# Performance work log

Hardware: AMD Instinct MI355X
Metric: run time of the kernel (lower is better)

The kernel has to match this reference:

```python
import jax, jax.numpy as jnp
import numpy as np

D_MODEL = 1024
NUM_HEADS = 16
DEPTH = D_MODEL // NUM_HEADS


def setup_inputs() -> dict:
    key = jax.random.key(0)
    ks = jax.random.split(key, 11)
    B, S = 2, 2048
    s = 1.0 / np.sqrt(D_MODEL)
    inp = {
        'query': jax.random.normal(ks[0], (B, S, D_MODEL), jnp.float32),
        'key': jax.random.normal(ks[1], (B, S, D_MODEL), jnp.float32),
        'value': jax.random.normal(ks[2], (B, S, D_MODEL), jnp.float32),
        'Wq': jax.random.normal(ks[3], (D_MODEL, D_MODEL), jnp.float32) * s,
        'bq': jnp.zeros((D_MODEL,), jnp.float32),
        'Wk': jax.random.normal(ks[4], (D_MODEL, D_MODEL), jnp.float32) * s,
        'bk': jnp.zeros((D_MODEL,), jnp.float32),
        'Wv': jax.random.normal(ks[5], (D_MODEL, D_MODEL), jnp.float32) * s,
        'bv': jnp.zeros((D_MODEL,), jnp.float32),
        'Wo': jax.random.normal(ks[6], (D_MODEL, D_MODEL), jnp.float32) * s,
        'bo': jnp.zeros((D_MODEL,), jnp.float32),
    }
    return inp


def reference(query, key, value, Wq, bq, Wk, bk, Wv, bv, Wo, bo):
    B, S, _ = query.shape
    # QKV projections (nn.Linear: x @ W.T + b; here W stored as [in,out])
    Q = query @ Wq + bq
    K = key @ Wk + bk
    V = value @ Wv + bv
    # [B, H, S, depth]
    Q = Q.reshape(B, S, NUM_HEADS, DEPTH).transpose(0, 2, 1, 3)
    K = K.reshape(B, S, NUM_HEADS, DEPTH).transpose(0, 2, 1, 3)
    V = V.reshape(B, S, NUM_HEADS, DEPTH).transpose(0, 2, 1, 3)
    scores = jnp.einsum('bhqd,bhkd->bhqk', Q, K) / jnp.sqrt(jnp.float32(DEPTH))
    weights = jax.nn.softmax(scores, axis=-1)
    out = jnp.einsum('bhqk,bhkd->bhqd', weights, V)
    out = out.transpose(0, 2, 1, 3).reshape(B, S, D_MODEL)
    return out @ Wo + bo
```

## Files before the change

kernel.cpp:

```cpp
#include <hip/hip_runtime.h>
#include <stdint.h>

#define D_MODEL 1024
#define NHEAD   16
#define DEPTH   64
#define BATCH   2
#define SEQ     2048
#define M_ROWS  (BATCH*SEQ)

typedef __attribute__((ext_vector_type(8))) short short8;
typedef __attribute__((ext_vector_type(4))) float f32x4;
typedef _Float16 __attribute__((ext_vector_type(8))) half8;
typedef __fp16 __attribute__((ext_vector_type(2))) fp16x2;

__device__ __forceinline__ unsigned short f2b(float f) {
    union { float f; uint32_t u; } v; v.f = f;
    uint32_t r = (v.u + 0x7FFFu + ((v.u >> 16) & 1u)) >> 16;
    return (unsigned short)r;
}
__device__ __forceinline__ unsigned short f2h(float f) {
    union { _Float16 h; unsigned short u; } c; c.h = (_Float16)f; return c.u;
}
__device__ __forceinline__ unsigned int pkh(float a, float b) {
    union { fp16x2 h; unsigned int u; } c;
    c.h = __builtin_amdgcn_cvt_pkrtz(a, b);
    return c.u;
}
__device__ __forceinline__ float exp2fast(float x) {
#if defined(__has_builtin) && __has_builtin(__builtin_amdgcn_exp2f)
    return __builtin_amdgcn_exp2f(x);
#else
    return exp2f(x);
#endif
}

__device__ __forceinline__ void glds16(const void* g, void* l) {
    __builtin_amdgcn_global_load_lds(
        (const __attribute__((address_space(1))) unsigned int*)(uintptr_t)g,
        (__attribute__((address_space(3))) unsigned int*)(unsigned int)(uintptr_t)l,
        16, 0, 0);
}

__global__ __launch_bounds__(256) void cast3_bf16(
    const float* __restrict__ s0, const float* __restrict__ s1, const float* __restrict__ s2,
    unsigned short* __restrict__ d0, unsigned short* __restrict__ d1, unsigned short* __restrict__ d2)
{
    const float* s; unsigned short* d;
    if (blockIdx.y == 0)      { s = s0; d = d0; }
    else if (blockIdx.y == 1) { s = s1; d = d1; }
    else                      { s = s2; d = d2; }
    int i = blockIdx.x * 256 + threadIdx.x;
    float4 v = ((const float4*)s)[i];
    ushort4 u;
    u.x = f2b(v.x); u.y = f2b(v.y); u.z = f2b(v.z); u.w = f2b(v.w);
    ((ushort4*)d)[i] = u;
}

__global__ __launch_bounds__(256) void transpose_w(
    const float* __restrict__ w0, const float* __restrict__ w1,
    const float* __restrict__ w2, const float* __restrict__ w3,
    unsigned short* __restrict__ t0, unsigned short* __restrict__ t1,
    unsigned short* __restrict__ t2, unsigned short* __restrict__ t3)
{
    __shared__ unsigned short tile[64][65];
    const float* w; unsigned short* t;
    const int z = blockIdx.z;
    switch (z) {
        case 0:  w = w0; t = t0; break;
        case 1:  w = w1; t = t1; break;
        case 2:  w = w2; t = t2; break;
        default: w = w3; t = t3; break;
    }
    const float sc = (z == 0) ? 0.125f * 1.44269504089f : 1.0f;
    const int k0 = blockIdx.y * 64;
    const int n0 = blockIdx.x * 64;
    const int tid = threadIdx.x;
    #pragma unroll
    for (int i = 0; i < 16; ++i) {
        int idx = i * 256 + tid;
        int r = idx >> 6, c = idx & 63;
        tile[c][r] = f2b(w[(size_t)(k0 + r) * D_MODEL + n0 + c] * sc);
    }
    __syncthreads();
    #pragma unroll
    for (int i = 0; i < 16; ++i) {
        int idx = i * 256 + tid;
        int r = idx >> 6, c = idx & 63;
        t[(size_t)(n0 + r) * D_MODEL + k0 + c] = tile[r][c];
    }
}

template<int OUT_MODE, bool BIAS_M>
__device__ __forceinline__ void gemm_body(
    const unsigned short* __restrict__ A, const unsigned short* __restrict__ Bt,
    const float* __restrict__ bias, float bscale, void* __restrict__ Cv,
    int m0, int n0, int N, int K, unsigned short* As, unsigned short* Bs)
{
    const int tid  = threadIdx.x;
    const int lane = tid & 63;
    const int wave = tid >> 6;
    const int wm = wave & 1, wn = wave >> 1;
    const int quad = lane >> 4, l16 = lane & 15;

    auto stage = [&](int buf, int k0) {
        unsigned short* Ad = As + buf * (128 * 32);
        unsigned short* Bd = Bs + buf * (128 * 32);
        #pragma unroll
        for (int i = 0; i < 2; ++i) {
            int c = i * 256 + tid;
            int row = c >> 2, cb = c & 3;
            glds16(A  + (size_t)(m0 + row) * K + k0 + cb * 8, Ad + c * 8);
            glds16(Bt + (size_t)(n0 + row) * K + k0 + cb * 8, Bd + c * 8);
        }
    };

    f32x4 acc[4][4] = {};
    float bn[4];
    if (!BIAS_M) {
        #pragma unroll
        for (int nt = 0; nt < 4; ++nt) bn[nt] = bias[n0 + wn * 64 + nt * 16 + l16] * bscale;
    }

    stage(0, 0);
    const int NIT = K / 32;
    for (int it = 0; it < NIT; ++it) {
        __syncthreads();
        const unsigned short* Ab = As + (it & 1) * (128 * 32);
        const unsigned short* Bb = Bs + (it & 1) * (128 * 32);
        if (it + 1 < NIT) stage((it + 1) & 1, (it + 1) * 32);
        short8 af[4], bg[4];
        #pragma unroll
        for (int t = 0; t < 4; ++t) {
            af[t] = *(const short8*)&Ab[(wm * 64 + t * 16 + l16) * 32 + quad * 8];
            bg[t] = *(const short8*)&Bb[(wn * 64 + t * 16 + l16) * 32 + quad * 8];
        }
        #pragma unroll
        for (int mt = 0; mt < 4; ++mt)
            #pragma unroll
            for (int nt = 0; nt < 4; ++nt)
                acc[mt][nt] = __builtin_amdgcn_mfma_f32_16x16x32_bf16(af[mt], bg[nt], acc[mt][nt], 0, 0, 0);
    }

    #pragma unroll
    for (int mt = 0; mt < 4; ++mt)
        #pragma unroll
        for (int nt = 0; nt < 4; ++nt)
            #pragma unroll
            for (int r = 0; r < 4; ++r) {
                int m = m0 + wm * 64 + mt * 16 + quad * 4 + r;
                int n = n0 + wn * 64 + nt * 16 + l16;
                float bv_ = BIAS_M ? bias[m] * bscale : bn[nt];
                float val = acc[mt][nt][r] + bv_;
                if (OUT_MODE == 1)      ((unsigned short*)Cv)[(size_t)m * N + n] = f2b(val);
                else if (OUT_MODE == 2) ((unsigned short*)Cv)[(size_t)m * N + n] = f2h(val);
                else                    ((float*)Cv)[(size_t)m * N + n] = val;
            }
}

__global__ __launch_bounds__(256, 3) void gemm_qkvt(
    const unsigned short* __restrict__ xq, const unsigned short* __restrict__ xk,
    const unsigned short* __restrict__ xv, const unsigned short* __restrict__ wT,
    const float* __restrict__ bq, const float* __restrict__ bk, const float* __restrict__ bv,
    unsigned short* __restrict__ Qb, unsigned short* __restrict__ Kb, unsigned short* __restrict__ Vtg)
{
    __shared__ __align__(16) unsigned short As[2 * 128 * 32];
    __shared__ __align__(16) unsigned short Bs[2 * 128 * 32];
    const int z = blockIdx.y, t = blockIdx.x;
    const size_t wn = (size_t)D_MODEL * D_MODEL;
    if (z < 2) {
        int m0 = (t >> 3) * 128, n0 = (t & 7) * 128;
        gemm_body<1, false>(z ? xk : xq, wT + z * wn, z ? bk : bq, z ? 1.0f : 0.125f * 1.44269504089f,
                            z ? Kb : Qb, m0, n0, D_MODEL, D_MODEL, As, Bs);
    } else {
        int m0 = (t & 7) * 128, n0 = (t >> 3) * 128;
        gemm_body<2, true>(wT + 2 * wn, xv, bv, 1.0f, Vtg, m0, n0, M_ROWS, D_MODEL, As, Bs);
    }
}

__global__ __launch_bounds__(256, 2) void gemm_out(
    const unsigned short* __restrict__ A, const unsigned short* __restrict__ Bt,
    const float* __restrict__ bias, float* __restrict__ C)
{
    __shared__ __align__(16) unsigned short As[2 * 128 * 32];
    __shared__ __align__(16) unsigned short Bs[2 * 64 * 32];
    const int tid  = threadIdx.x;
    const int lane = tid & 63;
    const int wave = tid >> 6;
    const int wm = wave & 1, wn = wave >> 1;
    const int quad = lane >> 4, l16 = lane & 15;
    const int m0 = (blockIdx.x >> 4) * 128, n0 = (blockIdx.x & 15) * 64;
    const int N = D_MODEL, K = D_MODEL;

    auto stage = [&](int buf, int k0) {
        unsigned short* Ad = As + buf * (128 * 32);
        unsigned short* Bd = Bs + buf * (64 * 32);
        #pragma unroll
        for (int i = 0; i < 2; ++i) {
            int c = i * 256 + tid;
            int row = c >> 2, cb = c & 3;
            glds16(A + (size_t)(m0 + row) * K + k0 + cb * 8, Ad + c * 8);
        }
        int c = tid, row = c >> 2, cb = c & 3;
        glds16(Bt + (size_t)(n0 + row) * K + k0 + cb * 8, Bd + c * 8);
    };

    f32x4 acc[4][2] = {};
    float bn[2];
    #pragma unroll
    for (int nt = 0; nt < 2; ++nt) bn[nt] = bias[n0 + wn * 32 + nt * 16 + l16];

    stage(0, 0);
    const int NIT = K / 32;
    for (int it = 0; it < NIT; ++it) {
        __syncthreads();
        const unsigned short* Ab = As + (it & 1) * (128 * 32);
        const unsigned short* Bb = Bs + (it & 1) * (64 * 32);
        if (it + 1 < NIT) stage((it + 1) & 1, (it + 1) * 32);
        short8 af[4], bg[2];
        #pragma unroll
        for (int t = 0; t < 4; ++t)
            af[t] = *(const short8*)&Ab[(wm * 64 + t * 16 + l16) * 32 + quad * 8];
        #pragma unroll
        for (int t = 0; t < 2; ++t)
            bg[t] = *(const short8*)&Bb[(wn * 32 + t * 16 + l16) * 32 + quad * 8];
        #pragma unroll
        for (int mt = 0; mt < 4; ++mt)
            #pragma unroll
            for (int nt = 0; nt < 2; ++nt)
                acc[mt][nt] = __builtin_amdgcn_mfma_f32_16x16x32_bf16(af[mt], bg[nt], acc[mt][nt], 0, 0, 0);
    }

    #pragma unroll
    for (int mt = 0; mt < 4; ++mt)
        #pragma unroll
        for (int nt = 0; nt < 2; ++nt)
            #pragma unroll
            for (int r = 0; r < 4; ++r) {
                int m = m0 + wm * 64 + mt * 16 + quad * 4 + r;
                int n = n0 + wn * 32 + nt * 16 + l16;
                C[(size_t)m * N + n] = acc[mt][nt][r] + bn[nt];
            }
}

__global__ __launch_bounds__(128, 1) void attn_mfma(
    const unsigned short* __restrict__ Qb, const unsigned short* __restrict__ Kb,
    const unsigned short* __restrict__ Vtg, unsigned short* __restrict__ ctx)
{
    constexpr int PLD = 72;
    __shared__ __align__(16) unsigned short Ks[2][64 * 64];
    __shared__ __align__(16) unsigned short Vs[2][64 * 64];
    __shared__ __align__(16) unsigned short Ps[2][64 * PLD];

    const int tid = threadIdx.x, lane = tid & 63, wave = tid >> 6;
    const int quad = lane >> 4, l16 = lane & 15;
    const int b = blockIdx.z, h = blockIdx.y;
    const int q0 = blockIdx.x * 128 + wave * 64;
    unsigned short* Psw = Ps[wave];

    short8 bqf[4][2];
    #pragma unroll
    for (int nt = 0; nt < 4; ++nt)
        #pragma unroll
        for (int ks = 0; ks < 2; ++ks)
            bqf[nt][ks] = *(const short8*)(Qb +
                (size_t)(b * SEQ + q0 + nt * 16 + l16) * D_MODEL + h * DEPTH + ks * 32 + quad * 8);

    const unsigned short* Kbase = Kb  + (size_t)b * SEQ * D_MODEL + h * DEPTH;
    const unsigned short* Vbase = Vtg + (size_t)h * DEPTH * M_ROWS + (size_t)b * SEQ;

    auto stage = [&](int buf, int kt) {
        const unsigned short* Kt = Kbase + (size_t)kt * 64 * D_MODEL;
        const unsigned short* Vt = Vbase + kt * 64;
        #pragma unroll
        for (int i = 0; i < 4; ++i) {
            int c = i * 128 + tid;
            int row = c >> 3, sj = (c & 7) ^ (row & 7);
            glds16(Kt + (size_t)row * D_MODEL + sj * 8, &Ks[buf][c * 8]);
            glds16(Vt + (size_t)row * M_ROWS  + sj * 8, &Vs[buf][c * 8]);
        }
    };

    const int x7 = l16 & 7;
    f32x4 o[4][4] = {};
    float lsum[4] = {0.f, 0.f, 0.f, 0.f};

    stage(0, 0);
    for (int kt = 0; kt < SEQ / 64; ++kt) {
        __syncthreads();
        const int buf = kt & 1;
        if (kt + 1 < SEQ / 64) stage(buf ^ 1, kt + 1);
        const unsigned short* Kf = Ks[buf];
        const unsigned short* Vf = Vs[buf];

        f32x4 s[4][4] = {};
        #pragma unroll
        for (int mt = 0; mt < 4; ++mt) {
            short8 ak[2];
            #pragma unroll
            for (int ks = 0; ks < 2; ++ks)
                ak[ks] = *(const short8*)&Kf[(mt * 16 + l16) * 64 + ((ks * 4 + quad) ^ x7) * 8];
            #pragma unroll
            for (int nt = 0; nt < 4; ++nt)
                #pragma unroll
                for (int ks = 0; ks < 2; ++ks)
                    s[mt][nt] = __builtin_amdgcn_mfma_f32_16x16x32_bf16(ak[ks], bqf[nt][ks], s[mt][nt], 0, 0, 0);
        }

        #pragma unroll
        for (int mt = 0; mt < 4; ++mt)
            #pragma unroll
            for (int nt = 0; nt < 4; ++nt) {
                float p0 = exp2fast(fminf(s[mt][nt][0], 14.4f));
                float p1 = exp2fast(fminf(s[mt][nt][1], 14.4f));
                float p2 = exp2fast(fminf(s[mt][nt][2], 14.4f));
                float p3 = exp2fast(fminf(s[mt][nt][3], 14.4f));
                lsum[nt] += (p0 + p1) + (p2 + p3);
                uint2 u; u.x = pkh(p0, p1); u.y = pkh(p2, p3);
                *(uint2*)&Psw[(nt * 16 + l16) * PLD + mt * 16 + quad * 4] = u;
            }

        #pragma unroll
        for (int ks = 0; ks < 2; ++ks) {
            half8 ap[4], bvf[4];
            #pragma unroll
            for (int mq = 0; mq < 4; ++mq)
                ap[mq] = *(const half8*)&Psw[(mq * 16 + l16) * PLD + ks * 32 + quad * 8];
            #pragma unroll
            for (int nd = 0; nd < 4; ++nd)
                bvf[nd] = *(const half8*)&Vf[(nd * 16 + l16) * 64 + ((ks * 4 + quad) ^ x7) * 8];
            #pragma unroll
            for (int mq = 0; mq < 4; ++mq)
                #pragma unroll
                for (int nd = 0; nd < 4; ++nd)
                    o[mq][nd] = __builtin_amdgcn_mfma_f32_16x16x32_f16(ap[mq], bvf[nd], o[mq][nd], 0, 0, 0);
        }
    }

    float linv[4];
    #pragma unroll
    for (int nt = 0; nt < 4; ++nt) {
        float t = lsum[nt];
        t += __shfl_xor(t, 16);
        t += __shfl_xor(t, 32);
        linv[nt] = 1.0f / t;
    }
    #pragma unroll
    for (int mq = 0; mq < 4; ++mq)
        #pragma unroll
        for (int r = 0; r < 4; ++r) {
            float li = __shfl(linv[mq], quad * 4 + r);
            #pragma unroll
            for (int nd = 0; nd < 4; ++nd)
                ctx[(size_t)(b * SEQ + q0 + mq * 16 + quad * 4 + r) * D_MODEL +
                    h * DEPTH + nd * 16 + l16] = f2b(o[mq][nd][r] * li);
        }
}

extern "C" void kernel_launch(void* const* d_in, const int* in_sizes, int n_in,
                              void* d_out, int out_size, void* d_ws, size_t ws_size,
                              hipStream_t stream)
{
    const float* query = (const float*)d_in[0];
    const float* key   = (const float*)d_in[1];
    const float* value = (const float*)d_in[2];
    const float* Wq = (const float*)d_in[3];
    const float* bq = (const float*)d_in[4];
    const float* Wk = (const float*)d_in[5];
    const float* bk = (const float*)d_in[6];
    const float* Wv = (const float*)d_in[7];
    const float* bv = (const float*)d_in[8];
    const float* Wo = (const float*)d_in[9];
    const float* bo = (const float*)d_in[10];

    char* ws = (char*)d_ws;
    size_t off = 0;
    auto alloc = [&](size_t bytes) -> char* {
        char* p = ws + off;
        off += (bytes + 255) & ~(size_t)255;
        return p;
    };
    const size_t xn = (size_t)M_ROWS * D_MODEL;
    const size_t wn = (size_t)D_MODEL * D_MODEL;
    unsigned short* xq   = (unsigned short*)alloc(xn * 2);
    unsigned short* xk   = (unsigned short*)alloc(xn * 2);
    unsigned short* xv   = (unsigned short*)alloc(xn * 2);
    unsigned short* wT   = (unsigned short*)alloc(3 * wn * 2);
    unsigned short* woT  = (unsigned short*)alloc(wn * 2);
    unsigned short* Qb   = (unsigned short*)alloc(xn * 2);
    unsigned short* Kb   = (unsigned short*)alloc(xn * 2);
    unsigned short* Vtg  = (unsigned short*)alloc(xn * 2);
    unsigned short* ctx  = (unsigned short*)alloc(xn * 2);
    if (off > ws_size) return;

    cast3_bf16<<<dim3(4096, 3), 256, 0, stream>>>(query, key, value, xq, xk, xv);
    transpose_w<<<dim3(16, 16, 4), 256, 0, stream>>>(
        Wq, Wk, Wv, Wo, wT, wT + wn, wT + 2 * wn, woT);
    gemm_qkvt<<<dim3(256, 3), 256, 0, stream>>>(xq, xk, xv, wT, bq, bk, bv, Qb, Kb, Vtg);
    attn_mfma<<<dim3(SEQ / 128, NHEAD, BATCH), 128, 0, stream>>>(Qb, Kb, Vtg, ctx);
    gemm_out<<<dim3(512), 256, 0, stream>>>(ctx, woT, bo, (float*)d_out);
}
```

Measured before the change: 234.9 us.

## Split attention blocks into four 32-query waves and fuse prep kernels

The attention kernel now runs 256 threads per block with four waves of 32 queries each, in place of two waves of 64. This halves per-wave accumulator and score registers so occupancy can rise (launch bounds 256,3), and each K/V tile is shared by more waves. The P scratch buffer switches from padded rows to an XOR-swizzled layout to avoid LDS bank conflicts, and the staging loads are redistributed per wave. Separately, the cast and weight-transpose kernels are merged into one launch to save a kernel launch. The trade-off is more MFMA issue overhead per query and more contention for LDS and barriers.

```diff
diff --git a/kernel.cpp b/kernel.cpp
--- a/kernel.cpp
+++ b/kernel.cpp
@@ -41,52 +41,50 @@
         16, 0, 0);
 }
 
-__global__ __launch_bounds__(256) void cast3_bf16(
-    const float* __restrict__ s0, const float* __restrict__ s1, const float* __restrict__ s2,
-    unsigned short* __restrict__ d0, unsigned short* __restrict__ d1, unsigned short* __restrict__ d2)
-{
-    const float* s; unsigned short* d;
-    if (blockIdx.y == 0)      { s = s0; d = d0; }
-    else if (blockIdx.y == 1) { s = s1; d = d1; }
-    else                      { s = s2; d = d2; }
-    int i = blockIdx.x * 256 + threadIdx.x;
-    float4 v = ((const float4*)s)[i];
-    ushort4 u;
-    u.x = f2b(v.x); u.y = f2b(v.y); u.z = f2b(v.z); u.w = f2b(v.w);
-    ((ushort4*)d)[i] = u;
-}
-
-__global__ __launch_bounds__(256) void transpose_w(
+__global__ __launch_bounds__(256) void prep(
+    const float* __restrict__ q, const float* __restrict__ k, const float* __restrict__ v,
+    unsigned short* __restrict__ xq, unsigned short* __restrict__ xk, unsigned short* __restrict__ xv,
     const float* __restrict__ w0, const float* __restrict__ w1,
     const float* __restrict__ w2, const float* __restrict__ w3,
     unsigned short* __restrict__ t0, unsigned short* __restrict__ t1,
     unsigned short* __restrict__ t2, unsigned short* __restrict__ t3)
 {
     __shared__ unsigned short tile[64][65];
-    const float* w; unsigned short* t;
-    const int z = blockIdx.z;
-    switch (z) {
-        case 0:  w = w0; t = t0; break;
-        case 1:  w = w1; t = t1; break;
-        case 2:  w = w2; t = t2; break;
-        default: w = w3; t = t3; break;
-    }
-    const float sc = (z == 0) ? 0.125f * 1.44269504089f : 1.0f;
-    const int k0 = blockIdx.y * 64;
-    const int n0 = blockIdx.x * 64;
-    const int tid = threadIdx.x;
-    #pragma unroll
-    for (int i = 0; i < 16; ++i) {
-        int idx = i * 256 + tid;
-        int r = idx >> 6, c = idx & 63;
-        tile[c][r] = f2b(w[(size_t)(k0 + r) * D_MODEL + n0 + c] * sc);
-    }
-    __syncthreads();
-    #pragma unroll
-    for (int i = 0; i < 16; ++i) {
-        int idx = i * 256 + tid;
-        int r = idx >> 6, c = idx & 63;
-        t[(size_t)(n0 + r) * D_MODEL + k0 + c] = tile[r][c];
+    const int bid = blockIdx.x, tid = threadIdx.x;
+    if (bid < 12288) {
+        const int t = bid >> 12;
+        const float* s = (t == 0) ? q : (t == 1) ? k : v;
+        unsigned short* d = (t == 0) ? xq : (t == 1) ? xk : xv;
+        int i = (bid & 4095) * 256 + tid;
+        float4 val = ((const float4*)s)[i];
+        ushort4 u;
+        u.x = f2b(val.x); u.y = f2b(val.y); u.z = f2b(val.z); u.w = f2b(val.w);
+        ((ushort4*)d)[i] = u;
+    } else {
+        const int r3 = bid - 12288;
+        const int z = r3 >> 8, by = (r3 & 255) >> 4, bx = r3 & 15;
+        const float* w; unsigned short* t;
+        switch (z) {
+            case 0:  w = w0; t = t0; break;
+            case 1:  w = w1; t = t1; break;
+            case 2:  w = w2; t = t2; break;
+            default: w = w3; t = t3; break;
+        }
+        const float sc = (z == 0) ? 0.125f * 1.44269504089f : 1.0f;
+        const int k0 = by * 64, n0 = bx * 64;
+        #pragma unroll
+        for (int i = 0; i < 16; ++i) {
+            int idx = i * 256 + tid;
+            int r = idx >> 6, c = idx & 63;
+            tile[c][r] = f2b(w[(size_t)(k0 + r) * D_MODEL + n0 + c] * sc);
+        }
+        __syncthreads();
+        #pragma unroll
+        for (int i = 0; i < 16; ++i) {
+            int idx = i * 256 + tid;
+            int r = idx >> 6, c = idx & 63;
+            t[(size_t)(n0 + r) * D_MODEL + k0 + c] = tile[r][c];
+        }
     }
 }
 
@@ -242,24 +240,23 @@
             }
 }
 
-__global__ __launch_bounds__(128, 1) void attn_mfma(
+__global__ __launch_bounds__(256, 3) void attn_mfma(
     const unsigned short* __restrict__ Qb, const unsigned short* __restrict__ Kb,
     const unsigned short* __restrict__ Vtg, unsigned short* __restrict__ ctx)
 {
-    constexpr int PLD = 72;
     __shared__ __align__(16) unsigned short Ks[2][64 * 64];
     __shared__ __align__(16) unsigned short Vs[2][64 * 64];
-    __shared__ __align__(16) unsigned short Ps[2][64 * PLD];
+    __shared__ __align__(16) unsigned short Ps[4][32 * 64];
 
     const int tid = threadIdx.x, lane = tid & 63, wave = tid >> 6;
     const int quad = lane >> 4, l16 = lane & 15;
     const int b = blockIdx.z, h = blockIdx.y;
-    const int q0 = blockIdx.x * 128 + wave * 64;
+    const int q0 = blockIdx.x * 128 + wave * 32;
     unsigned short* Psw = Ps[wave];
 
-    short8 bqf[4][2];
-    #pragma unroll
-    for (int nt = 0; nt < 4; ++nt)
+    short8 bqf[2][2];
+    #pragma unroll
+    for (int nt = 0; nt < 2; ++nt)
         #pragma unroll
         for (int ks = 0; ks < 2; ++ks)
             bqf[nt][ks] = *(const short8*)(Qb +
@@ -268,21 +265,23 @@
     const unsigned short* Kbase = Kb  + (size_t)b * SEQ * D_MODEL + h * DEPTH;
     const unsigned short* Vbase = Vtg + (size_t)h * DEPTH * M_ROWS + (size_t)b * SEQ;
 
+    const int srow = lane >> 3;
+    const int schunk = (lane & 7) ^ srow;
     auto stage = [&](int buf, int kt) {
         const unsigned short* Kt = Kbase + (size_t)kt * 64 * D_MODEL;
         const unsigned short* Vt = Vbase + kt * 64;
         #pragma unroll
-        for (int i = 0; i < 4; ++i) {
-            int c = i * 128 + tid;
-            int row = c >> 3, sj = (c & 7) ^ (row & 7);
-            glds16(Kt + (size_t)row * D_MODEL + sj * 8, &Ks[buf][c * 8]);
-            glds16(Vt + (size_t)row * M_ROWS  + sj * 8, &Vs[buf][c * 8]);
+        for (int i = 0; i < 2; ++i) {
+            int g = i * 4 + wave;
+            int row = g * 8 + srow;
+            glds16(Kt + (size_t)row * D_MODEL + schunk * 8, &Ks[buf][g * 512 + lane * 8]);
+            glds16(Vt + (size_t)row * M_ROWS  + schunk * 8, &Vs[buf][g * 512 + lane * 8]);
         }
     };
 
     const int x7 = l16 & 7;
-    f32x4 o[4][4] = {};
-    float lsum[4] = {0.f, 0.f, 0.f, 0.f};
+    f32x4 o[2][4] = {};
+    float lsum[2] = {0.f, 0.f};
 
     stage(0, 0);
     for (int kt = 0; kt < SEQ / 64; ++kt) {
@@ -292,7 +291,7 @@
         const unsigned short* Kf = Ks[buf];
         const unsigned short* Vf = Vs[buf];
 
-        f32x4 s[4][4] = {};
+        f32x4 s[4][2] = {};
         #pragma unroll
         for (int mt = 0; mt < 4; ++mt) {
             short8 ak[2];
@@ -300,7 +299,7 @@
             for (int ks = 0; ks < 2; ++ks)
                 ak[ks] = *(const short8*)&Kf[(mt * 16 + l16) * 64 + ((ks * 4 + quad) ^ x7) * 8];
             #pragma unroll
-            for (int nt = 0; nt < 4; ++nt)
+            for (int nt = 0; nt < 2; ++nt)
                 #pragma unroll
                 for (int ks = 0; ks < 2; ++ks)
                     s[mt][nt] = __builtin_amdgcn_mfma_f32_16x16x32_bf16(ak[ks], bqf[nt][ks], s[mt][nt], 0, 0, 0);
@@ -309,43 +308,44 @@
         #pragma unroll
         for (int mt = 0; mt < 4; ++mt)
             #pragma unroll
-            for (int nt = 0; nt < 4; ++nt) {
+            for (int nt = 0; nt < 2; ++nt) {
                 float p0 = exp2fast(fminf(s[mt][nt][0], 14.4f));
                 float p1 = exp2fast(fminf(s[mt][nt][1], 14.4f));
                 float p2 = exp2fast(fminf(s[mt][nt][2], 14.4f));
                 float p3 = exp2fast(fminf(s[mt][nt][3], 14.4f));
                 lsum[nt] += (p0 + p1) + (p2 + p3);
                 uint2 u; u.x = pkh(p0, p1); u.y = pkh(p2, p3);
-                *(uint2*)&Psw[(nt * 16 + l16) * PLD + mt * 16 + quad * 4] = u;
+                *(uint2*)&Psw[(nt * 16 + l16) * 64 +
+                              (((mt * 2 + (quad >> 1)) ^ x7) * 8 + (quad & 1) * 4)] = u;
             }
 
         #pragma unroll
         for (int ks = 0; ks < 2; ++ks) {
-            half8 ap[4], bvf[4];
-            #pragma unroll
-            for (int mq = 0; mq < 4; ++mq)
-                ap[mq] = *(const half8*)&Psw[(mq * 16 + l16) * PLD + ks * 32 + quad * 8];
+            half8 ap[2], bvf[4];
+            #pragma unroll
+            for (int mq = 0; mq < 2; ++mq)
+                ap[mq] = *(const half8*)&Psw[(mq * 16 + l16) * 64 + ((ks * 4 + quad) ^ x7) * 8];
             #pragma unroll
             for (int nd = 0; nd < 4; ++nd)
                 bvf[nd] = *(const half8*)&Vf[(nd * 16 + l16) * 64 + ((ks * 4 + quad) ^ x7) * 8];
             #pragma unroll
-            for (int mq = 0; mq < 4; ++mq)
+            for (int mq = 0; mq < 2; ++mq)
                 #pragma unroll
                 for (int nd = 0; nd < 4; ++nd)
                     o[mq][nd] = __builtin_amdgcn_mfma_f32_16x16x32_f16(ap[mq], bvf[nd], o[mq][nd], 0, 0, 0);
         }
     }
 
-    float linv[4];
-    #pragma unroll
-    for (int nt = 0; nt < 4; ++nt) {
+    float linv[2];
+    #pragma unroll
+    for (int nt = 0; nt < 2; ++nt) {
         float t = lsum[nt];
         t += __shfl_xor(t, 16);
         t += __shfl_xor(t, 32);
         linv[nt] = 1.0f / t;
     }
     #pragma unroll
-    for (int mq = 0; mq < 4; ++mq)
+    for (int mq = 0; mq < 2; ++mq)
         #pragma unroll
         for (int r = 0; r < 4; ++r) {
             float li = __shfl(linv[mq], quad * 4 + r);
@@ -392,10 +392,10 @@
     unsigned short* ctx  = (unsigned short*)alloc(xn * 2);
     if (off > ws_size) return;
 
-    cast3_bf16<<<dim3(4096, 3), 256, 0, stream>>>(query, key, value, xq, xk, xv);
-    transpose_w<<<dim3(16, 16, 4), 256, 0, stream>>>(
+    prep<<<dim3(13312), 256, 0, stream>>>(
+        query, key, value, xq, xk, xv,
         Wq, Wk, Wv, Wo, wT, wT + wn, wT + 2 * wn, woT);
     gemm_qkvt<<<dim3(256, 3), 256, 0, stream>>>(xq, xk, xv, wT, bq, bk, bv, Qb, Kb, Vtg);
-    attn_mfma<<<dim3(SEQ / 128, NHEAD, BATCH), 128, 0, stream>>>(Qb, Kb, Vtg, ctx);
+    attn_mfma<<<dim3(SEQ / 128, NHEAD, BATCH), 256, 0, stream>>>(Qb, Kb, Vtg, ctx);
     gemm_out<<<dim3(512), 256, 0, stream>>>(ctx, woT, bo, (float*)d_out);
 }
```

Measured after the change: 225.7 us. 1.04x faster.
